# Optimization experiments

Measured on AMD Instinct MI355X. Metric: run time of the kernel, lower is better.

The kernel has to match this reference:

```python
import jax, jax.numpy as jnp
import numpy as np
from jax import lax

SIGMA = 0.2
SPACING = 3
EPS = 1e-8

def multinomial_pool(prob, key, spacing=SPACING):
    """Stochastic multinomial max-pool over spacing x spacing blocks.
    Returns (sparse_detection [B,C,H,W], pooled_map [B,C,H/s,W/s], winner [B,C,H/s,W/s] int)."""
    B, C, H, W = prob.shape
    s = spacing
    Hb, Wb = H // s, W // s
    # [B,C,Hb,Wb,s*s]
    blocks = prob.reshape(B, C, Hb, s, Wb, s).transpose(0, 1, 2, 4, 3, 5).reshape(B, C, Hb, Wb, s * s)
    logits = jnp.log(blocks + EPS)
    g = jax.random.gumbel(key, blocks.shape, dtype=prob.dtype)
    winner = jnp.argmax(logits + g, axis=-1)                      # [B,C,Hb,Wb]
    onehot = jax.nn.one_hot(winner, s * s, dtype=prob.dtype)      # [B,C,Hb,Wb,s*s]
    sparse_blocks = blocks * onehot
    pooled = jnp.sum(sparse_blocks, axis=-1)                      # prob at winner
    sparse = sparse_blocks.reshape(B, C, Hb, Wb, s, s).transpose(0, 1, 2, 4, 3, 5).reshape(B, C, H, W)
    return sparse, pooled, winner

def crbm_layer(x, W, b, key):
    pre = lax.conv_general_dilated(x, W, window_strides=(1, 1), padding='VALID',
                                   dimension_numbers=('NCHW', 'OIHW', 'NCHW'))
    pre = (pre + b[None, :, None, None]) / (SIGMA ** 2)
    prob = jax.nn.sigmoid(pre)
    _, pooled, _ = multinomial_pool(prob, key)
    return pooled

def setup_inputs() -> dict:
    key = jax.random.key(0)
    kx, k1, k2 = jax.random.split(key, 3)
    x = jax.random.uniform(kx, (64, 3, 96, 96), dtype=jnp.float32)
    W1 = jax.random.normal(k1, (96, 3, 7, 7), dtype=jnp.float32) * 0.1
    b1 = jnp.zeros((96,), dtype=jnp.float32)
    W2 = jax.random.normal(k2, (192, 96, 7, 7), dtype=jnp.float32) * 0.1
    b2 = jnp.zeros((192,), dtype=jnp.float32)
    return {"x": x, "W1": W1, "b1": b1, "W2": W2, "b2": b2}

def reference(x, W1, b1, W2, b2):
    key = jax.random.key(42)
    kp1, kp2 = jax.random.split(key)
    h1 = crbm_layer(x, W1, b1, kp1)    # [64,96,30,30]
    h2 = crbm_layer(h1, W2, b2, kp2)   # [64,192,8,8]
    return h2
```

## Files before the change

kernel.cpp:

```cpp
#include <hip/hip_runtime.h>
#include <cstdint>
#include <math.h>


#define EPS_D 1e-8
#define INV_SIGMA2 (1.0 / (0.2 * 0.2))
#define TAU 6e-3
#define TAU1 2e-3f
#define REDO_CAP 32768
#define H1_BYTES (5529600ull * 8ull)
#define H1F32_BYTES (5529600ull * 4ull)
#define CONV_BYTES (64ull * 576ull * 192ull * 4ull)
#define WSPLIT_ELEMS (49ull * 192ull * 96ull)
#define XSPL_PLANE 2359296ull
#define XSPL_BYTES (3ull * XSPL_PLANE * 2ull)
#define W1B_ELEMS (7ull * 3ull * 96ull * 32ull)

typedef __bf16 bf16x8 __attribute__((ext_vector_type(8)));
typedef __bf16 bf16x4 __attribute__((ext_vector_type(4)));
typedef float f32x4 __attribute__((ext_vector_type(4)));

#define MFMA(A_, B_, C_) \
  __builtin_amdgcn_mfma_f32_16x16x32_bf16((A_), (B_), (C_), 0, 0, 0)

__host__ __device__ __forceinline__ void threefry2x32(
    uint32_t k0, uint32_t k1, uint32_t x0, uint32_t x1,
    uint32_t* o0, uint32_t* o1) {
  const uint32_t ks0 = k0, ks1 = k1, ks2 = k0 ^ k1 ^ 0x1BD11BDAu;
  x0 += ks0; x1 += ks1;
#define TF_R(r) { x0 += x1; x1 = (x1 << (r)) | (x1 >> (32 - (r))); x1 ^= x0; }
  TF_R(13) TF_R(15) TF_R(26) TF_R(6)
  x0 += ks1; x1 += ks2 + 1u;
  TF_R(17) TF_R(29) TF_R(16) TF_R(24)
  x0 += ks2; x1 += ks0 + 2u;
  TF_R(13) TF_R(15) TF_R(26) TF_R(6)
  x0 += ks0; x1 += ks1 + 3u;
  TF_R(17) TF_R(29) TF_R(16) TF_R(24)
  x0 += ks1; x1 += ks2 + 4u;
  TF_R(13) TF_R(15) TF_R(26) TF_R(6)
  x0 += ks2; x1 += ks0 + 5u;
#undef TF_R
  *o0 = x0; *o1 = x1;
}

__device__ __forceinline__ double fast_log(double x) {
  long long ib = __double_as_longlong(x);
  int e = (int)((ib >> 52) & 0x7ff) - 1023;
  double r = __longlong_as_double((ib & 0xfffffffffffffLL) | 0x3ff0000000000000LL);
  if (r > 1.4142135623730951) { r *= 0.5; e += 1; }
  double s = (r - 1.0) / (r + 1.0);
  double s2 = s * s;
  double t = fma(s2, fma(s2, fma(s2, fma(s2, fma(s2, fma(s2,
      1.0/15.0, 1.0/13.0), 1.0/11.0), 1.0/9.0), 1.0/7.0), 1.0/5.0), 1.0/3.0);
  double lr = fma(2.0 * s * s2, t, 2.0 * s);
  return fma((double)e, 0.6931471805599453, lr);
}

__device__ __forceinline__ double fast_exp(double x) {
  double nd = rint(x * 1.4426950408889634);
  double f = fma(nd, -0.6931471803691238, x);
  f = fma(nd, -1.9082149292705877e-10, f);
  double p = 2.505210838544172e-8;
  p = fma(p, f, 2.755731922398589e-7);
  p = fma(p, f, 2.7557319223985893e-6);
  p = fma(p, f, 2.48015873015873e-5);
  p = fma(p, f, 1.984126984126984e-4);
  p = fma(p, f, 1.3888888888888889e-3);
  p = fma(p, f, 8.333333333333333e-3);
  p = fma(p, f, 4.1666666666666664e-2);
  p = fma(p, f, 0.16666666666666666);
  p = fma(p, f, 0.5);
  p = fma(p, f, 1.0);
  p = fma(p, f, 1.0);
  return ldexp(p, (int)nd);
}

__device__ __forceinline__ double gumbel_pool9(const double (&acc)[9],
                                               double bb, uint64_t base,
                                               uint32_t kp0, uint32_t kp1) {
  double bestv = -1e308, bA = 1.0, bQ = 0.0;
#pragma unroll
  for (int k = 0; k < 9; ++k) {
    double pre = (acc[k] + bb) * INV_SIGMA2;
    double q = fast_exp(-fabs(pre));
    double A = pre >= 0.0 ? 1.0 : q;
    double opq = 1.0 + q;
    double L = fast_log(fma(EPS_D, opq, A)) - fast_log(opq);
    uint32_t o0, o1;
    uint64_t idx = base + (uint64_t)k;
    threefry2x32(kp0, kp1, (uint32_t)(idx >> 32), (uint32_t)idx, &o0, &o1);
    uint32_t bits = o0 ^ o1;
    float u = __uint_as_float((bits >> 9) | 0x3f800000u) - 1.0f;
    if (u == 0.0f) u = 1.17549435e-38f;
    float lg1 = (float)fast_log((double)u);
    double lg2 = fast_log(-(double)lg1);
    float gf = -(float)lg2;
    double v = L + (double)gf;
    if (v > bestv) { bestv = v; bA = A; bQ = q; }
  }
  return bA / (1.0 + bQ);
}

__device__ __forceinline__ double gumbel_pool9_gap(const double (&acc)[9],
                                                   double bb, uint64_t base,
                                                   uint32_t kp0, uint32_t kp1,
                                                   double* gap) {
  double bestv = -1e308, second = -1e308, bA = 1.0, bQ = 0.0;
#pragma unroll
  for (int k = 0; k < 9; ++k) {
    double pre = (acc[k] + bb) * INV_SIGMA2;
    double q = fast_exp(-fabs(pre));
    double A = pre >= 0.0 ? 1.0 : q;
    double opq = 1.0 + q;
    double L = fast_log(fma(EPS_D, opq, A)) - fast_log(opq);
    uint32_t o0, o1;
    uint64_t idx = base + (uint64_t)k;
    threefry2x32(kp0, kp1, (uint32_t)(idx >> 32), (uint32_t)idx, &o0, &o1);
    uint32_t bits = o0 ^ o1;
    float u = __uint_as_float((bits >> 9) | 0x3f800000u) - 1.0f;
    if (u == 0.0f) u = 1.17549435e-38f;
    float lg1 = (float)fast_log((double)u);
    double lg2 = fast_log(-(double)lg1);
    float gf = -(float)lg2;
    double v = L + (double)gf;
    if (v > bestv) { second = bestv; bestv = v; bA = A; bQ = q; }
    else if (v > second) second = v;
  }
  *gap = bestv - second;
  return bA / (1.0 + bQ);
}

__device__ __forceinline__ float gumbel_pool9_gap_f32(
    const float (&acc)[9], float bb, uint64_t base,
    uint32_t kp0, uint32_t kp1, float* gap) {
  float bestv = -1e30f, second = -1e30f, bA = 1.0f, bQ = 0.0f;
#pragma unroll
  for (int k = 0; k < 9; ++k) {
    float pre = (acc[k] + bb) * 25.0f;
    float q = __expf(-fabsf(pre));
    float A = pre >= 0.0f ? 1.0f : q;
    float opq = 1.0f + q;
    float L = __logf(fmaf(1e-8f, opq, A)) - __logf(opq);
    uint32_t o0, o1;
    uint64_t idx = base + (uint64_t)k;
    threefry2x32(kp0, kp1, (uint32_t)(idx >> 32), (uint32_t)idx, &o0, &o1);
    uint32_t bits = o0 ^ o1;
    float u = __uint_as_float((bits >> 9) | 0x3f800000u) - 1.0f;
    if (u == 0.0f) u = 1.17549435e-38f;
    float lg1 = __logf(u);
    float gf = -__logf(-lg1);
    float v = L + gf;
    if (v > bestv) { second = bestv; bestv = v; bA = A; bQ = q; }
    else if (v > second) second = v;
  }
  *gap = bestv - second;
  return bA / (1.0f + bQ);
}

__device__ __forceinline__ unsigned short f32_to_bf16(float v) {
  uint32_t u = __float_as_uint(v);
  return (unsigned short)((u + 0x7fffu + ((u >> 16) & 1u)) >> 16);
}
__device__ __forceinline__ float bf16_to_f32(unsigned short s) {
  return __uint_as_float(((uint32_t)s) << 16);
}

template <int LDSTRIDE, typename T>
__device__ __forceinline__ void conv_pair(const T* __restrict__ xb,
                                          const double (&w)[49],
                                          double (&a0)[9], double (&a1)[9]) {
#pragma unroll
  for (int pr = 0; pr < 12; ++pr) {
    double xr[9];
#pragma unroll
    for (int c = 0; c < 9; ++c) xr[c] = (double)xb[pr * LDSTRIDE + c];
#pragma unroll
    for (int ki = 0; ki < 3; ++ki) {
      const int u0 = pr - ki;
      if (u0 >= 0 && u0 <= 6) {
#pragma unroll
        for (int kj = 0; kj < 3; ++kj)
#pragma unroll
          for (int v = 0; v < 7; ++v)
            a0[ki * 3 + kj] = fma(xr[kj + v], w[u0 * 7 + v], a0[ki * 3 + kj]);
      }
      const int u1 = pr - 3 - ki;
      if (u1 >= 0 && u1 <= 6) {
#pragma unroll
        for (int kj = 0; kj < 3; ++kj)
#pragma unroll
          for (int v = 0; v < 7; ++v)
            a1[ki * 3 + kj] = fma(xr[kj + v], w[u1 * 7 + v], a1[ki * 3 + kj]);
      }
    }
  }
}

__global__ void init_cnt_kernel(unsigned int* __restrict__ cnt) {
  cnt[0] = 0u; cnt[1] = 0u;
}

__global__ __launch_bounds__(256, 3) void l1_kernel(
    const float* __restrict__ x, const float* __restrict__ W1,
    const float* __restrict__ b1, double* __restrict__ h1,
    float* __restrict__ h1f32, int write_f64, int write_f32,
    unsigned int* __restrict__ cnt, uint32_t kp0, uint32_t kp1) {
  const int oc   = blockIdx.x;
  const int b    = blockIdx.y;
  const int half = blockIdx.z;
  const int t = threadIdx.x;
  const int wave = t >> 6;

  if (cnt && oc == 0 && b == 0 && half == 0 && t == 0) *cnt = 0u;

  __shared__ float xs[54 * 96];

  const int p0 = 14 * half;
  const bool active = t < 240;
  const int q = t / 30, bw = t - q * 30;
  const float* xb = xs + (6 * q) * 96 + 3 * bw;

  double a0[9] = {}, a1[9] = {};
  double w[49];

#pragma unroll 1
  for (int ic = 0; ic < 3; ++ic) {
    __syncthreads();
    {
      const char* gsrc = (const char*)(x + ((size_t)b * 3 + ic) * 9216 + (3 * p0) * 96);
#pragma unroll
      for (int p = 0; p < 6; ++p) {
        int elt = p * 256 + t;
        if (elt < 1296) {
          __builtin_amdgcn_global_load_lds(
              (const __attribute__((address_space(1))) void*)(gsrc + (size_t)elt * 16),
              (__attribute__((address_space(3))) void*)((char*)xs +
                                                        (size_t)(p * 256 + wave * 64) * 16),
              16, 0, 0);
        }
      }
    }
    __syncthreads();
    {
      const float* __restrict__ wsrc = W1 + (oc * 3 + ic) * 49;
#pragma unroll
      for (int j = 0; j < 49; ++j) w[j] = (double)wsrc[j];
    }
    if (active) conv_pair<96, float>(xb, w, a0, a1);
  }

  if (active) {
    const double bb = (double)b1[oc];
    const int bh0 = p0 + 2 * q;
#pragma unroll
    for (int j = 0; j < 2; ++j) {
      const int pos = (bh0 + j) * 30 + bw;
      const uint64_t base = ((uint64_t)((b * 96 + oc) * 900 + pos)) * 9ull;
      double pooled = gumbel_pool9(j ? a1 : a0, bb, base, kp0, kp1);
      const size_t oidx = (size_t)(b * 96 + oc) * 900 + pos;
      if (write_f64) h1[oidx] = pooled;
      if (write_f32) h1f32[oidx] = (float)pooled;
    }
  }
}

__global__ __launch_bounds__(256) void x_split_kernel(
    const float* __restrict__ x, unsigned short* __restrict__ xs) {
  int idx = blockIdx.x * 256 + threadIdx.x;
  int px = idx % 96; int rest = idx / 96;
  int row = rest % 96; int b = rest / 96;
  unsigned long long pk[3] = {0ull, 0ull, 0ull};
#pragma unroll
  for (int ic = 0; ic < 3; ++ic) {
    float v = x[((size_t)(b * 3 + ic) * 96 + row) * 96 + px];
    unsigned short s0 = f32_to_bf16(v); float r1 = v - bf16_to_f32(s0);
    unsigned short s1 = f32_to_bf16(r1); float r2 = r1 - bf16_to_f32(s1);
    unsigned short s2 = f32_to_bf16(r2);
    pk[0] |= (unsigned long long)s0 << (16 * ic);
    pk[1] |= (unsigned long long)s1 << (16 * ic);
    pk[2] |= (unsigned long long)s2 << (16 * ic);
  }
#pragma unroll
  for (int p = 0; p < 3; ++p)
    *(unsigned long long*)(xs + (size_t)p * XSPL_PLANE + (size_t)idx * 4) = pk[p];
}

__global__ __launch_bounds__(256) void w1_split_kernel(
    const float* __restrict__ W1, unsigned short* __restrict__ wb) {
  int idx = blockIdx.x * 256 + threadIdx.x;
  int k = idx % 32; int rest = idx / 32;
  int oc = rest % 96; int kh = rest / 96;
  int kw = k >> 2, ic = k & 3;
  float v = (ic < 3 && kw < 7) ? W1[(((size_t)oc * 3 + ic) * 7 + kh) * 7 + kw] : 0.0f;
  unsigned short a = f32_to_bf16(v); float r1 = v - bf16_to_f32(a);
  unsigned short b = f32_to_bf16(r1); float r2 = r1 - bf16_to_f32(b);
  unsigned short c = f32_to_bf16(r2);
  wb[((size_t)(kh * 3 + 0) * 96 + oc) * 32 + k] = a;
  wb[((size_t)(kh * 3 + 1) * 96 + oc) * 32 + k] = b;
  wb[((size_t)(kh * 3 + 2) * 96 + oc) * 32 + k] = c;
}

__global__ __launch_bounds__(256) void w2_split_kernel(
    const float* __restrict__ W2, unsigned short* __restrict__ s0,
    unsigned short* __restrict__ s1, unsigned short* __restrict__ s2) {
  int idx = blockIdx.x * 256 + threadIdx.x;
  int ic = idx % 96; int rest = idx / 96;
  int oc = rest % 192; int tap = rest / 192;
  float v = W2[(size_t)(oc * 96 + ic) * 49 + tap];
  unsigned short a = f32_to_bf16(v); float r1 = v - bf16_to_f32(a);
  unsigned short b = f32_to_bf16(r1); float r2 = r1 - bf16_to_f32(b);
  unsigned short c = f32_to_bf16(r2);
  s0[idx] = a; s1[idx] = b; s2[idx] = c;
}

__global__ __launch_bounds__(256, 2) void l1_mfma_kernel(
    const unsigned short* __restrict__ xs, const unsigned short* __restrict__ wb,
    const float* __restrict__ b1, float* __restrict__ h1f32,
    unsigned int* __restrict__ cnt, unsigned int* __restrict__ list,
    uint32_t kp0, uint32_t kp1) {
  const int xt = blockIdx.x;
  const int yt = blockIdx.y;
  const int b  = blockIdx.z;
  const int t = threadIdx.x;
  const int w = t >> 6;
  const int l = t & 63;
  const int g = l >> 4;
  const int lr = l & 15;
  const int x0 = 30 * xt;
  const int y0 = 6 * yt;

  __shared__ __align__(16) float smem_f[17640];
  char* smem = (char*)smem_f;

  if (t < 4) smem_f[2592 + t] = 0.0f;

  {
    const int wave64 = w << 6;
#pragma unroll
    for (int p = 0; p < 3; ++p) {
      int s = p * 256 + t;
      if (s < 648) {
        int pl = s / 216;
        int r2 = s - pl * 216;
        int row = r2 / 18;
        int ch = r2 - row * 18;
        const char* src = (const char*)(xs + (size_t)pl * XSPL_PLANE +
                          ((size_t)((b * 96 + y0 + row) * 96 + x0)) * 4) + ch * 16;
        __builtin_amdgcn_global_load_lds(
            (const __attribute__((address_space(1))) void*)src,
            (__attribute__((address_space(3))) void*)(smem + (size_t)(p * 256 + wave64) * 16),
            16, 0, 0);
      }
    }
  }

  int aoff[3];
#pragma unroll
  for (int mf = 0; mf < 3; ++mf) {
    int pos = (w * 3 + mf) * 16 + lr;
    if (pos > 179) pos = 179;
    int ya = pos / 30, xxa = pos - 30 * ya;
    aoff[mf] = ya * 288 + xxa * 8 + g * 16;
  }

  f32x4 acc[3][6];
#pragma unroll
  for (int mf = 0; mf < 3; ++mf)
#pragma unroll
    for (int nf = 0; nf < 6; ++nf) acc[mf][nf] = (f32x4){0.f, 0.f, 0.f, 0.f};

  __syncthreads();

#pragma unroll 1
  for (int kh = 0; kh < 7; ++kh) {
    bf16x8 bc[6][3];
#pragma unroll
    for (int nf = 0; nf < 6; ++nf) {
      int oc = nf * 16 + lr;
#pragma unroll
      for (int pl = 0; pl < 3; ++pl)
        bc[nf][pl] = *(const bf16x8*)&wb[(((size_t)kh * 3 + pl) * 96 + oc) * 32 + 8 * g];
    }
#pragma unroll
    for (int mf = 0; mf < 3; ++mf) {
      const char* ap = smem + kh * 288 + aoff[mf];
      bf16x4 a0l = *(const bf16x4*)(ap);
      bf16x4 a0h = *(const bf16x4*)(ap + 8);
      bf16x4 a1l = *(const bf16x4*)(ap + 3456);
      bf16x4 a1h = *(const bf16x4*)(ap + 3464);
      bf16x4 a2l = *(const bf16x4*)(ap + 6912);
      bf16x4 a2h = *(const bf16x4*)(ap + 6920);
      bf16x8 a0 = __builtin_shufflevector(a0l, a0h, 0, 1, 2, 3, 4, 5, 6, 7);
      bf16x8 a1 = __builtin_shufflevector(a1l, a1h, 0, 1, 2, 3, 4, 5, 6, 7);
      bf16x8 a2 = __builtin_shufflevector(a2l, a2h, 0, 1, 2, 3, 4, 5, 6, 7);
#pragma unroll
      for (int nf = 0; nf < 6; ++nf) {
        f32x4 c = acc[mf][nf];
        c = MFMA(a0, bc[nf][0], c);
        c = MFMA(a0, bc[nf][1], c);
        c = MFMA(a1, bc[nf][0], c);
        c = MFMA(a1, bc[nf][1], c);
        c = MFMA(a0, bc[nf][2], c);
        c = MFMA(a2, bc[nf][0], c);
        acc[mf][nf] = c;
      }
    }
  }

  __syncthreads();
  {
#pragma unroll
    for (int mf = 0; mf < 3; ++mf)
#pragma unroll
      for (int nf = 0; nf < 6; ++nf)
#pragma unroll
        for (int r = 0; r < 4; ++r) {
          int pos = (w * 3 + mf) * 16 + g * 4 + r;
          if (pos < 180) smem_f[pos * 98 + nf * 16 + lr] = acc[mf][nf][r];
        }
  }
  __syncthreads();

#pragma unroll 1
  for (int i = 0; i < 8; ++i) {
    int oi = i * 256 + t;
    if (oi < 1920) {
      int oc = oi % 96; int rc = oi / 96;
      int pc = rc % 10, pr = rc / 10;
      float a[9];
      float chk = 0.0f;
#pragma unroll
      for (int dy = 0; dy < 3; ++dy)
#pragma unroll
        for (int dx = 0; dx < 3; ++dx) {
          float v = smem_f[((pr * 3 + dy) * 30 + pc * 3 + dx) * 98 + oc];
          a[dy * 3 + dx] = v;
          chk += v;
        }
      int gy = yt * 2 + pr, gx = xt * 10 + pc;
      unsigned int oidx = (unsigned int)((b * 96 + oc) * 900 + gy * 30 + gx);
      float gap;
      float pooled = gumbel_pool9_gap_f32(a, b1[oc], (uint64_t)oidx * 9ull,
                                          kp0, kp1, &gap);
      h1f32[oidx] = pooled;
      if (!(gap >= TAU1) || chk != chk) {
        unsigned int idx = atomicAdd(cnt, 1u);
        if (idx < REDO_CAP) list[idx] = oidx;
      }
    }
  }
}

__global__ __launch_bounds__(64) void l1_redo_kernel(
    const float* __restrict__ x, const float* __restrict__ W1,
    const float* __restrict__ b1, float* __restrict__ h1f32,
    const unsigned int* __restrict__ cnt, const unsigned int* __restrict__ list,
    uint32_t kp0, uint32_t kp1) {
  unsigned int n = *cnt;
  if (n > REDO_CAP) n = REDO_CAP;
  if (blockIdx.x >= n) return;
  const unsigned int oidx = list[blockIdx.x];
  const int gx = oidx % 30;
  const int gy = (oidx / 30) % 30;
  const int rest = oidx / 900;
  const int oc = rest % 96, b = rest / 96;
  const int lane = threadIdx.x;

  double acc[9] = {};
  if (lane < 49) {
    const int kh = lane / 7, kw = lane % 7;
#pragma unroll
    for (int ic = 0; ic < 3; ++ic) {
      double wv = (double)W1[(((size_t)oc * 3 + ic) * 7 + kh) * 7 + kw];
      const float* __restrict__ xp = x + ((size_t)(b * 3 + ic) * 96) * 96;
#pragma unroll
      for (int dy = 0; dy < 3; ++dy)
#pragma unroll
        for (int dx = 0; dx < 3; ++dx) {
          int y = 3 * gy + dy + kh, xc = 3 * gx + dx + kw;
          acc[dy * 3 + dx] = fma((double)xp[(size_t)y * 96 + xc], wv, acc[dy * 3 + dx]);
        }
    }
  }
#pragma unroll
  for (int off = 32; off; off >>= 1)
#pragma unroll
    for (int k = 0; k < 9; ++k) acc[k] += __shfl_down(acc[k], off);

  if (lane == 0) {
    double pooled = gumbel_pool9(acc, (double)b1[oc], (uint64_t)oidx * 9ull,
                                 kp0, kp1);
    h1f32[oidx] = (float)pooled;
  }
}

__global__ __launch_bounds__(256, 1) void l2_mfma_kernel(
    const float* __restrict__ h1f32, const unsigned short* __restrict__ wp0,
    const unsigned short* __restrict__ wp1,
    const unsigned short* __restrict__ wp2, float* __restrict__ conv) {
  const int nt = blockIdx.x;
  const int my = blockIdx.y;
  const int b = my / 3, mt = my - 3 * b;
  const int t = threadIdx.x;
  const int l = t & 63;
  const int w = t >> 6;
  const int wm = w >> 1, wn = w & 1;
  const int g = l >> 4;
  const int lr = l & 15;

  __shared__ unsigned short As[3 * 4 * 14 * 30 * 8];

  int rowoff[6];
#pragma unroll
  for (int mf = 0; mf < 6; ++mf) {
    int ml = wm * 96 + mf * 16 + lr;
    int yl = ml / 24, xx = ml - 24 * yl;
    rowoff[mf] = g * 3360 + (yl * 30 + xx) * 8;
  }
  const int oc0 = nt * 64 + wn * 32 + lr;

  f32x4 acc[6][2];
#pragma unroll
  for (int mf = 0; mf < 6; ++mf)
#pragma unroll
    for (int nf = 0; nf < 2; ++nf) acc[mf][nf] = (f32x4){0.f, 0.f, 0.f, 0.f};

#pragma unroll 1
  for (int ch = 0; ch < 3; ++ch) {
    __syncthreads();
    {
      const float* __restrict__ hb =
          h1f32 + ((size_t)b * 96 + ch * 32) * 900 + (8 * mt) * 30;
#pragma unroll 1
      for (int idx = t; idx < 13440; idx += 256) {
        int i = idx / 420, rem = idx - i * 420;
        float v = hb[(size_t)i * 900 + rem];
        unsigned short p0 = f32_to_bf16(v);
        float r1 = v - bf16_to_f32(p0);
        unsigned short p1 = f32_to_bf16(r1);
        float r2 = r1 - bf16_to_f32(p1);
        unsigned short p2 = f32_to_bf16(r2);
        int base = (i >> 3) * 3360 + rem * 8 + (i & 7);
        As[base] = p0; As[base + 13440] = p1; As[base + 26880] = p2;
      }
    }
    __syncthreads();

    int boff = oc0 * 96 + ch * 32 + 8 * g;
    bf16x8 bc[2][3], bn[2][3];
#pragma unroll
    for (int nf = 0; nf < 2; ++nf) {
      bc[nf][0] = *(const bf16x8*)&wp0[boff + nf * 1536];
      bc[nf][1] = *(const bf16x8*)&wp1[boff + nf * 1536];
      bc[nf][2] = *(const bf16x8*)&wp2[boff + nf * 1536];
    }
    int kh = 0, kw = 0;
#pragma unroll 1
    for (int tap = 0; tap < 49; ++tap) {
      if (tap < 48) {
        const int bo2 = boff + 18432;
#pragma unroll
        for (int nf = 0; nf < 2; ++nf) {
          bn[nf][0] = *(const bf16x8*)&wp0[bo2 + nf * 1536];
          bn[nf][1] = *(const bf16x8*)&wp1[bo2 + nf * 1536];
          bn[nf][2] = *(const bf16x8*)&wp2[bo2 + nf * 1536];
        }
        boff = bo2;
      }
      const int tapoff = (kh * 30 + kw) * 8;
#pragma unroll
      for (int mf = 0; mf < 6; ++mf) {
        const int ab = rowoff[mf] + tapoff;
        bf16x8 a0 = *(const bf16x8*)&As[ab];
        bf16x8 a1 = *(const bf16x8*)&As[ab + 13440];
        bf16x8 a2 = *(const bf16x8*)&As[ab + 26880];
#pragma unroll
        for (int nf = 0; nf < 2; ++nf) {
          f32x4 c = acc[mf][nf];
          c = MFMA(a0, bc[nf][0], c);
          c = MFMA(a0, bc[nf][1], c);
          c = MFMA(a1, bc[nf][0], c);
          c = MFMA(a1, bc[nf][1], c);
          c = MFMA(a0, bc[nf][2], c);
          c = MFMA(a2, bc[nf][0], c);
          acc[mf][nf] = c;
        }
      }
      if (tap < 48) {
#pragma unroll
        for (int nf = 0; nf < 2; ++nf)
#pragma unroll
          for (int s = 0; s < 3; ++s) bc[nf][s] = bn[nf][s];
      }
      if (++kw == 7) { kw = 0; ++kh; }
    }
  }

  const int rowsub = g * 4;
#pragma unroll
  for (int mf = 0; mf < 6; ++mf)
#pragma unroll
    for (int nf = 0; nf < 2; ++nf)
#pragma unroll
      for (int r = 0; r < 4; ++r) {
        const int m_abs = mt * 192 + wm * 96 + mf * 16 + rowsub + r;
        const int oc = oc0 + nf * 16;
        conv[((size_t)b * 576 + m_abs) * 192 + oc] = acc[mf][nf][r];
      }
}

__global__ __launch_bounds__(192) void l2_pool_kernel(
    const float* __restrict__ conv, const float* __restrict__ b2,
    float* __restrict__ out, unsigned int* __restrict__ cnt,
    unsigned int* __restrict__ list, uint32_t kp0, uint32_t kp1) {
  const int pos = blockIdx.x;
  const int b = blockIdx.y;
  const int oc = threadIdx.x;
  const int ph = pos >> 3, pw = pos & 7;
  double a[9];
  double chk = 0.0;
  const float* __restrict__ cb = conv + (size_t)b * 576 * 192 + oc;
#pragma unroll
  for (int dy = 0; dy < 3; ++dy)
#pragma unroll
    for (int dx = 0; dx < 3; ++dx) {
      double v = (double)cb[((size_t)((3 * ph + dy) * 24 + 3 * pw + dx)) * 192];
      a[dy * 3 + dx] = v;
      chk += v;
    }
  const unsigned int oid = (unsigned int)((b * 192 + oc) * 64 + pos);
  double gap;
  double pooled = gumbel_pool9_gap(a, (double)b2[oc], (uint64_t)oid * 9ull,
                                   kp0, kp1, &gap);
  out[oid] = (float)pooled;
  if (!(gap >= TAU) || chk != chk) {
    unsigned int idx = atomicAdd(cnt, 1u);
    if (idx < REDO_CAP) list[idx] = oid;
  }
}

__global__ __launch_bounds__(256, 3) void l2_kernel_f64(
    const double* __restrict__ h1, const float* __restrict__ W2,
    const float* __restrict__ b2, float* __restrict__ out,
    uint32_t kp0, uint32_t kp1) {
  const int octile = blockIdx.x;
  const int b      = blockIdx.y;
  const int t = threadIdx.x;
  const int wave = t >> 6;
  const int oc_local = t >> 5;
  const int li = t & 31;
  const int bw = li & 7;
  const int ph = 2 * ((li >> 3) & 1) + (li >> 4);
  const int bh0 = 2 * ph;
  const int oc = octile * 8 + oc_local;

  __shared__ double hs[2][900];
  __shared__ double wsd[2][392];

  const double* __restrict__ hb = h1 + (size_t)b * 86400;
  const float* __restrict__ wg = W2 + (size_t)octile * 8 * 4704;

  double a0[9] = {}, a1[9] = {};
  double w[49];

  auto stage = [&](int c, int buf) {
    const char* gsrc = (const char*)(hb + (size_t)c * 900);
#pragma unroll
    for (int p = 0; p < 2; ++p) {
      int elt = p * 256 + t;
      if (elt < 450) {
        __builtin_amdgcn_global_load_lds(
            (const __attribute__((address_space(1))) void*)(gsrc + (size_t)elt * 16),
            (__attribute__((address_space(3))) void*)((char*)&hs[buf][0] +
                                                      (size_t)(p * 256 + wave * 64) * 16),
            16, 0, 0);
      }
    }
#pragma unroll
    for (int p = 0; p < 2; ++p) {
      int j = p * 256 + t;
      if (j < 392) {
        int oi = j / 49, rem = j - oi * 49;
        wsd[buf][j] = (double)wg[(size_t)oi * 4704 + c * 49 + rem];
      }
    }
  };

  stage(0, 0);
#pragma unroll 1
  for (int c = 0; c < 96; ++c) {
    __syncthreads();
    if (c + 1 < 96) stage(c + 1, (c + 1) & 1);
    {
      const double* __restrict__ wsrc = &wsd[c & 1][oc_local * 49];
#pragma unroll
      for (int j = 0; j < 49; ++j) w[j] = wsrc[j];
      const double* xb = &hs[c & 1][(6 * ph) * 30 + 3 * bw];
      conv_pair<30, double>(xb, w, a0, a1);
    }
  }

  const double bb = (double)b2[oc];
#pragma unroll
  for (int j = 0; j < 2; ++j) {
    const int bh = bh0 + j;
    const uint64_t base = ((uint64_t)(((b * 192 + oc) * 8 + bh) * 8 + bw)) * 9ull;
    double pooled = gumbel_pool9(j ? a1 : a0, bb, base, kp0, kp1);
    out[(size_t)(b * 192 + oc) * 64 + bh * 8 + bw] = (float)pooled;
  }
}

__global__ __launch_bounds__(64) void l2_redo_kernel(
    const float* __restrict__ h1f, const float* __restrict__ W2,
    const float* __restrict__ b2, float* __restrict__ out,
    const unsigned int* __restrict__ cnt, const unsigned int* __restrict__ list,
    uint32_t kp0, uint32_t kp1) {
  unsigned int n = *cnt;
  if (n > REDO_CAP) n = REDO_CAP;
  if (blockIdx.x >= n) return;
  const unsigned int oid = list[blockIdx.x];
  const int sp = oid & 63, bh = sp >> 3, bw = sp & 7;
  const int rest = oid >> 6, oc = rest % 192, b = rest / 192;
  const int lane = threadIdx.x;

  double acc[9] = {};
  for (int ic = lane; ic < 96; ic += 64) {
    const float* __restrict__ xp =
        h1f + ((size_t)(b * 96 + ic) * 30 + 3 * bh) * 30 + 3 * bw;
    const float* __restrict__ wp = W2 + ((size_t)oc * 96 + ic) * 49;
    double w[49];
#pragma unroll
    for (int j = 0; j < 49; ++j) w[j] = (double)wp[j];
#pragma unroll
    for (int pr = 0; pr < 9; ++pr) {
      double xr[9];
#pragma unroll
      for (int c = 0; c < 9; ++c) xr[c] = (double)xp[pr * 30 + c];
#pragma unroll
      for (int kh = 0; kh < 3; ++kh) {
        const int u = pr - kh;
        if (u >= 0 && u <= 6) {
#pragma unroll
          for (int kw = 0; kw < 3; ++kw)
#pragma unroll
            for (int v = 0; v < 7; ++v)
              acc[kh * 3 + kw] = fma(xr[kw + v], w[u * 7 + v], acc[kh * 3 + kw]);
        }
      }
    }
  }
#pragma unroll
  for (int off = 32; off; off >>= 1)
#pragma unroll
    for (int k = 0; k < 9; ++k) acc[k] += __shfl_down(acc[k], off);

  if (lane == 0) {
    const uint64_t base = (uint64_t)oid * 9ull;
    double pooled = gumbel_pool9(acc, (double)b2[oc], base, kp0, kp1);
    out[oid] = (float)pooled;
  }
}

extern "C" void kernel_launch(void* const* d_in, const int* in_sizes, int n_in,
                              void* d_out, int out_size, void* d_ws,
                              size_t ws_size, hipStream_t stream) {
  const float* x  = (const float*)d_in[0];
  const float* W1 = (const float*)d_in[1];
  const float* b1 = (const float*)d_in[2];
  const float* W2 = (const float*)d_in[3];
  const float* b2 = (const float*)d_in[4];
  float* out = (float*)d_out;

  uint32_t kp1a, kp1b, kp2a, kp2b;
  threefry2x32(0u, 42u, 0u, 0u, &kp1a, &kp1b);
  threefry2x32(0u, 42u, 0u, 1u, &kp2a, &kp2b);

  const size_t WSPL_BYTES = WSPLIT_ELEMS * 2ull;
  const size_t need_main = H1F32_BYTES + CONV_BYTES + 3 * WSPL_BYTES +
                           16 + 2 * (size_t)REDO_CAP * 4;
  const size_t need_f64  = H1_BYTES;

  if (ws_size >= need_main) {
    char* wsb = (char*)d_ws;
    float* h1f32 = (float*)wsb;
    char* ub = wsb + H1F32_BYTES;
    unsigned short* xsplit = (unsigned short*)ub;
    unsigned short* w1b = (unsigned short*)(ub + XSPL_BYTES);
    float* conv = (float*)ub;
    unsigned short* wp0 = (unsigned short*)(ub + CONV_BYTES);
    unsigned short* wp1 = wp0 + WSPLIT_ELEMS;
    unsigned short* wp2 = wp1 + WSPLIT_ELEMS;
    unsigned int* cntblk = (unsigned int*)(ub + CONV_BYTES + 3 * WSPL_BYTES);
    unsigned int* list1 = cntblk + 4;
    unsigned int* list2 = list1 + REDO_CAP;

    init_cnt_kernel<<<1, 1, 0, stream>>>(cntblk);
    x_split_kernel<<<2304, 256, 0, stream>>>(x, xsplit);
    w1_split_kernel<<<84, 256, 0, stream>>>(W1, w1b);
    w2_split_kernel<<<3528, 256, 0, stream>>>(W2, wp0, wp1, wp2);
    l1_mfma_kernel<<<dim3(3, 15, 64), 256, 0, stream>>>(
        xsplit, w1b, b1, h1f32, cntblk + 0, list1, kp1a, kp1b);
    l1_redo_kernel<<<REDO_CAP, 64, 0, stream>>>(x, W1, b1, h1f32,
                                                cntblk + 0, list1, kp1a, kp1b);
    l2_mfma_kernel<<<dim3(3, 192), 256, 0, stream>>>(h1f32, wp0, wp1, wp2, conv);
    l2_pool_kernel<<<dim3(64, 64), 192, 0, stream>>>(conv, b2, out,
                                                     cntblk + 1, list2, kp2a, kp2b);
    l2_redo_kernel<<<REDO_CAP, 64, 0, stream>>>(h1f32, W2, b2, out,
                                                cntblk + 1, list2, kp2a, kp2b);
  } else {
    double* h1 = (double*)d_ws;
    l1_kernel<<<dim3(96, 64, 2), 256, 0, stream>>>(
        x, W1, b1, h1, (float*)0, 1, 0, (unsigned int*)0, kp1a, kp1b);
    l2_kernel_f64<<<dim3(24, 64), 256, 0, stream>>>(h1, W2, b2, out,
                                                    kp2a, kp2b);
  }
}
```

Before: 932.4 us.

## Emit channel-last bf16 split of h1 in layer 1 and stream it into LDS

Layer 1 now also writes its pooled output as a two-plane bf16 hi/lo split in NHWC layout. Layer 2 then loads tiles straight into LDS with global_load_lds instead of converting fp32 to three bf16 planes per block. The third split term and one MFMA per step are dropped. Occupancy is raised to 3 blocks per CU, and layer 2 runs in two batch halves so the conv scratch fits alongside the new buffer. This cuts per-block conversion work, LDS footprint and MFMA count, at the cost of lower precision in the layer-2 product (mitigated by the redo path) and extra global writes in layer 1.

```diff
diff --git a/kernel.cpp b/kernel.cpp
--- a/kernel.cpp
+++ b/kernel.cpp
@@ -10,11 +10,14 @@
 #define REDO_CAP 32768
 #define H1_BYTES (5529600ull * 8ull)
 #define H1F32_BYTES (5529600ull * 4ull)
-#define CONV_BYTES (64ull * 576ull * 192ull * 4ull)
+#define HB16_PLANE 5529600ull
+#define HB16_BYTES (2ull * HB16_PLANE * 2ull)
+#define CONVH_BYTES (32ull * 576ull * 192ull * 4ull)
 #define WSPLIT_ELEMS (49ull * 192ull * 96ull)
 #define XSPL_PLANE 2359296ull
 #define XSPL_BYTES (3ull * XSPL_PLANE * 2ull)
-#define W1B_ELEMS (7ull * 3ull * 96ull * 32ull)
+#define W1B_BYTES (7ull * 3ull * 96ull * 32ull * 2ull)
+#define RUNION_BYTES (XSPL_BYTES + W1B_BYTES)
 
 typedef __bf16 bf16x8 __attribute__((ext_vector_type(8)));
 typedef __bf16 bf16x4 __attribute__((ext_vector_type(4)));
@@ -316,6 +319,7 @@
 __global__ __launch_bounds__(256, 2) void l1_mfma_kernel(
     const unsigned short* __restrict__ xs, const unsigned short* __restrict__ wb,
     const float* __restrict__ b1, float* __restrict__ h1f32,
+    unsigned short* __restrict__ hb16,
     unsigned int* __restrict__ cnt, unsigned int* __restrict__ list,
     uint32_t kp0, uint32_t kp1) {
   const int xt = blockIdx.x;
@@ -438,11 +442,18 @@
           chk += v;
         }
       int gy = yt * 2 + pr, gx = xt * 10 + pc;
-      unsigned int oidx = (unsigned int)((b * 96 + oc) * 900 + gy * 30 + gx);
+      int pos = gy * 30 + gx;
+      unsigned int oidx = (unsigned int)((b * 96 + oc) * 900 + pos);
       float gap;
       float pooled = gumbel_pool9_gap_f32(a, b1[oc], (uint64_t)oidx * 9ull,
                                           kp0, kp1, &gap);
       h1f32[oidx] = pooled;
+      unsigned short s0 = f32_to_bf16(pooled);
+      float r1 = pooled - bf16_to_f32(s0);
+      unsigned short s1 = f32_to_bf16(r1);
+      size_t nidx = ((size_t)b * 900 + pos) * 96 + oc;
+      hb16[nidx] = s0;
+      hb16[HB16_PLANE + nidx] = s1;
       if (!(gap >= TAU1) || chk != chk) {
         unsigned int idx = atomicAdd(cnt, 1u);
         if (idx < REDO_CAP) list[idx] = oidx;
@@ -454,6 +465,7 @@
 __global__ __launch_bounds__(64) void l1_redo_kernel(
     const float* __restrict__ x, const float* __restrict__ W1,
     const float* __restrict__ b1, float* __restrict__ h1f32,
+    unsigned short* __restrict__ hb16,
     const unsigned int* __restrict__ cnt, const unsigned int* __restrict__ list,
     uint32_t kp0, uint32_t kp1) {
   unsigned int n = *cnt;
@@ -490,32 +502,43 @@
   if (lane == 0) {
     double pooled = gumbel_pool9(acc, (double)b1[oc], (uint64_t)oidx * 9ull,
                                  kp0, kp1);
-    h1f32[oidx] = (float)pooled;
-  }
-}
-
-__global__ __launch_bounds__(256, 1) void l2_mfma_kernel(
-    const float* __restrict__ h1f32, const unsigned short* __restrict__ wp0,
+    float pf = (float)pooled;
+    h1f32[oidx] = pf;
+    unsigned short s0 = f32_to_bf16(pf);
+    float r1 = pf - bf16_to_f32(s0);
+    unsigned short s1 = f32_to_bf16(r1);
+    size_t nidx = ((size_t)b * 900 + gy * 30 + gx) * 96 + oc;
+    hb16[nidx] = s0;
+    hb16[HB16_PLANE + nidx] = s1;
+  }
+}
+
+__global__ __launch_bounds__(256, 3) void l2_mfma_kernel(
+    const unsigned short* __restrict__ hb16,
+    const unsigned short* __restrict__ wp0,
     const unsigned short* __restrict__ wp1,
-    const unsigned short* __restrict__ wp2, float* __restrict__ conv) {
+    const unsigned short* __restrict__ wp2, float* __restrict__ conv,
+    int b_base) {
   const int nt = blockIdx.x;
   const int my = blockIdx.y;
-  const int b = my / 3, mt = my - 3 * b;
+  const int b_local = my / 3, mt = my - 3 * b_local;
+  const int b = b_base + b_local;
   const int t = threadIdx.x;
   const int l = t & 63;
   const int w = t >> 6;
   const int wm = w >> 1, wn = w & 1;
   const int g = l >> 4;
   const int lr = l & 15;
-
-  __shared__ unsigned short As[3 * 4 * 14 * 30 * 8];
+  const int wave64 = w << 6;
+
+  __shared__ __align__(16) unsigned short As2[2 * 4 * 420 * 8];
 
   int rowoff[6];
 #pragma unroll
   for (int mf = 0; mf < 6; ++mf) {
     int ml = wm * 96 + mf * 16 + lr;
     int yl = ml / 24, xx = ml - 24 * yl;
-    rowoff[mf] = g * 3360 + (yl * 30 + xx) * 8;
+    rowoff[mf] = g * 6720 + (yl * 30 + xx) * 16;
   }
   const int oc0 = nt * 64 + wn * 32 + lr;
 
@@ -524,24 +547,27 @@
   for (int mf = 0; mf < 6; ++mf)
 #pragma unroll
     for (int nf = 0; nf < 2; ++nf) acc[mf][nf] = (f32x4){0.f, 0.f, 0.f, 0.f};
+
+  const size_t pixbase = ((size_t)b * 900 + 240 * (size_t)mt) * 96;
 
 #pragma unroll 1
   for (int ch = 0; ch < 3; ++ch) {
     __syncthreads();
-    {
-      const float* __restrict__ hb =
-          h1f32 + ((size_t)b * 96 + ch * 32) * 900 + (8 * mt) * 30;
-#pragma unroll 1
-      for (int idx = t; idx < 13440; idx += 256) {
-        int i = idx / 420, rem = idx - i * 420;
-        float v = hb[(size_t)i * 900 + rem];
-        unsigned short p0 = f32_to_bf16(v);
-        float r1 = v - bf16_to_f32(p0);
-        unsigned short p1 = f32_to_bf16(r1);
-        float r2 = r1 - bf16_to_f32(p1);
-        unsigned short p2 = f32_to_bf16(r2);
-        int base = (i >> 3) * 3360 + rem * 8 + (i & 7);
-        As[base] = p0; As[base + 13440] = p1; As[base + 26880] = p2;
+#pragma unroll
+    for (int i = 0; i < 14; ++i) {
+      int s = i * 256 + t;
+      if (s < 3360) {
+        int pl = s / 1680;
+        int r = s - pl * 1680;
+        int g2 = r / 420;
+        int px = r - g2 * 420;
+        const unsigned short* src = hb16 + (size_t)pl * HB16_PLANE + pixbase +
+                                    (size_t)px * 96 + ch * 32 + g2 * 8;
+        __builtin_amdgcn_global_load_lds(
+            (const __attribute__((address_space(1))) void*)src,
+            (__attribute__((address_space(3))) void*)((char*)As2 +
+                                                      (size_t)(i * 256 + wave64) * 16),
+            16, 0, 0);
       }
     }
     __syncthreads();
@@ -567,13 +593,12 @@
         }
         boff = bo2;
       }
-      const int tapoff = (kh * 30 + kw) * 8;
+      const int tapoff = (kh * 30 + kw) * 16;
 #pragma unroll
       for (int mf = 0; mf < 6; ++mf) {
-        const int ab = rowoff[mf] + tapoff;
-        bf16x8 a0 = *(const bf16x8*)&As[ab];
-        bf16x8 a1 = *(const bf16x8*)&As[ab + 13440];
-        bf16x8 a2 = *(const bf16x8*)&As[ab + 26880];
+        const char* ap = (const char*)As2 + rowoff[mf] + tapoff;
+        bf16x8 a0 = *(const bf16x8*)(ap);
+        bf16x8 a1 = *(const bf16x8*)(ap + 26880);
 #pragma unroll
         for (int nf = 0; nf < 2; ++nf) {
           f32x4 c = acc[mf][nf];
@@ -582,7 +607,6 @@
           c = MFMA(a1, bc[nf][0], c);
           c = MFMA(a1, bc[nf][1], c);
           c = MFMA(a0, bc[nf][2], c);
-          c = MFMA(a2, bc[nf][0], c);
           acc[mf][nf] = c;
         }
       }
@@ -605,21 +629,22 @@
       for (int r = 0; r < 4; ++r) {
         const int m_abs = mt * 192 + wm * 96 + mf * 16 + rowsub + r;
         const int oc = oc0 + nf * 16;
-        conv[((size_t)b * 576 + m_abs) * 192 + oc] = acc[mf][nf][r];
+        conv[((size_t)b_local * 576 + m_abs) * 192 + oc] = acc[mf][nf][r];
       }
 }
 
 __global__ __launch_bounds__(192) void l2_pool_kernel(
     const float* __restrict__ conv, const float* __restrict__ b2,
     float* __restrict__ out, unsigned int* __restrict__ cnt,
-    unsigned int* __restrict__ list, uint32_t kp0, uint32_t kp1) {
+    unsigned int* __restrict__ list, uint32_t kp0, uint32_t kp1, int b_base) {
   const int pos = blockIdx.x;
-  const int b = blockIdx.y;
+  const int bl = blockIdx.y;
+  const int b = b_base + bl;
   const int oc = threadIdx.x;
   const int ph = pos >> 3, pw = pos & 7;
   double a[9];
   double chk = 0.0;
-  const float* __restrict__ cb = conv + (size_t)b * 576 * 192 + oc;
+  const float* __restrict__ cb = conv + (size_t)bl * 576 * 192 + oc;
 #pragma unroll
   for (int dy = 0; dy < 3; ++dy)
 #pragma unroll
@@ -776,21 +801,22 @@
   threefry2x32(0u, 42u, 0u, 1u, &kp2a, &kp2b);
 
   const size_t WSPL_BYTES = WSPLIT_ELEMS * 2ull;
-  const size_t need_main = H1F32_BYTES + CONV_BYTES + 3 * WSPL_BYTES +
-                           16 + 2 * (size_t)REDO_CAP * 4;
+  const size_t need_main = H1F32_BYTES + HB16_BYTES + RUNION_BYTES +
+                           3 * WSPL_BYTES + 16 + 2 * (size_t)REDO_CAP * 4;
   const size_t need_f64  = H1_BYTES;
 
   if (ws_size >= need_main) {
     char* wsb = (char*)d_ws;
     float* h1f32 = (float*)wsb;
-    char* ub = wsb + H1F32_BYTES;
-    unsigned short* xsplit = (unsigned short*)ub;
-    unsigned short* w1b = (unsigned short*)(ub + XSPL_BYTES);
-    float* conv = (float*)ub;
-    unsigned short* wp0 = (unsigned short*)(ub + CONV_BYTES);
+    unsigned short* hb16 = (unsigned short*)(wsb + H1F32_BYTES);
+    char* R = wsb + H1F32_BYTES + HB16_BYTES;
+    unsigned short* xsplit = (unsigned short*)R;
+    unsigned short* w1b = (unsigned short*)(R + XSPL_BYTES);
+    float* conv = (float*)R;
+    unsigned short* wp0 = (unsigned short*)(R + RUNION_BYTES);
     unsigned short* wp1 = wp0 + WSPLIT_ELEMS;
     unsigned short* wp2 = wp1 + WSPLIT_ELEMS;
-    unsigned int* cntblk = (unsigned int*)(ub + CONV_BYTES + 3 * WSPL_BYTES);
+    unsigned int* cntblk = (unsigned int*)(R + RUNION_BYTES + 3 * WSPL_BYTES);
     unsigned int* list1 = cntblk + 4;
     unsigned int* list2 = list1 + REDO_CAP;
 
@@ -799,12 +825,19 @@
     w1_split_kernel<<<84, 256, 0, stream>>>(W1, w1b);
     w2_split_kernel<<<3528, 256, 0, stream>>>(W2, wp0, wp1, wp2);
     l1_mfma_kernel<<<dim3(3, 15, 64), 256, 0, stream>>>(
-        xsplit, w1b, b1, h1f32, cntblk + 0, list1, kp1a, kp1b);
-    l1_redo_kernel<<<REDO_CAP, 64, 0, stream>>>(x, W1, b1, h1f32,
-                                                cntblk + 0, list1, kp1a, kp1b);
-    l2_mfma_kernel<<<dim3(3, 192), 256, 0, stream>>>(h1f32, wp0, wp1, wp2, conv);
-    l2_pool_kernel<<<dim3(64, 64), 192, 0, stream>>>(conv, b2, out,
-                                                     cntblk + 1, list2, kp2a, kp2b);
+        xsplit, w1b, b1, h1f32, hb16, cntblk + 0, list1, kp1a, kp1b);
+    l1_redo_kernel<<<REDO_CAP, 64, 0, stream>>>(
+        x, W1, b1, h1f32, hb16, cntblk + 0, list1, kp1a, kp1b);
+    l2_mfma_kernel<<<dim3(3, 96), 256, 0, stream>>>(hb16, wp0, wp1, wp2,
+                                                    conv, 0);
+    l2_pool_kernel<<<dim3(64, 32), 192, 0, stream>>>(conv, b2, out,
+                                                     cntblk + 1, list2,
+                                                     kp2a, kp2b, 0);
+    l2_mfma_kernel<<<dim3(3, 96), 256, 0, stream>>>(hb16, wp0, wp1, wp2,
+                                                    conv, 32);
+    l2_pool_kernel<<<dim3(64, 32), 192, 0, stream>>>(conv, b2, out,
+                                                     cntblk + 1, list2,
+                                                     kp2a, kp2b, 32);
     l2_redo_kernel<<<REDO_CAP, 64, 0, stream>>>(h1f32, W2, b2, out,
                                                 cntblk + 1, list2, kp2a, kp2b);
   } else {
```

Measured after the change: 961.7 us. +3.1%, slower.
